# Kernel tuning notes

Measured on AMD Instinct MI355X. Metric: run time of the kernel, lower is better.

Reference implementation:

```python
import jax, jax.numpy as jnp
import numpy as np

B, EMBED, HEADS, T = 2, 512, 8, 2048
DH = EMBED // HEADS
EPS = 1e-5
# NOTE: torch code computes embed_dim // num_heads ** 0.5 == 512 // sqrt(8)
SCALE = EMBED // HEADS ** 0.5  # = 181.0, reproduced faithfully


def ws_conv1x1(x, w, b, mask):
    # weight-standardized 1x1 conv; w: [O, I], x: [B, I, T], mask: [B, T]
    mu = jnp.mean(w, axis=1, keepdims=True)
    var = jnp.var(w, axis=1, keepdims=True)
    wn = (w - mu) * jax.lax.rsqrt(var + EPS)
    x = x * mask[:, None, :].astype(x.dtype)
    return jnp.einsum('oi,bit->bot', wn, x) + b[None, :, None]


def ln_head(x, g, b):
    # per-head LayerNorm over head dim; x: [B, H, DH, T], normalized over DH
    xt = jnp.swapaxes(x, -1, -2)  # [B, H, T, DH]
    mu = jnp.mean(xt, axis=-1, keepdims=True)
    var = jnp.var(xt, axis=-1, keepdims=True)
    xn = (xt - mu) * jax.lax.rsqrt(var + EPS) * g + b
    return jnp.swapaxes(xn, -1, -2)


def setup_inputs():
    key = jax.random.key(0)
    ks = jax.random.split(key, 12)
    sc = 1.0 / np.sqrt(EMBED)
    d = {
        'q': jax.random.normal(ks[0], (B, EMBED, T), jnp.float32),
        'k': jax.random.normal(ks[1], (B, EMBED, T), jnp.float32),
        'v': jax.random.normal(ks[2], (B, EMBED, T), jnp.float32),
        'query_mask': jax.random.randint(ks[3], (B, T), 0, 2, jnp.int32),
        'key_mask': jax.random.randint(ks[4], (B, T), 0, 2, jnp.int32),
        'value_mask': jax.random.randint(ks[5], (B, T), 0, 2, jnp.int32),
        'Wq': jax.random.normal(ks[6], (EMBED, EMBED), jnp.float32) * sc,
        'bq': jnp.zeros((EMBED,), jnp.float32),
        'Wk': jax.random.normal(ks[7], (EMBED, EMBED), jnp.float32) * sc,
        'bk': jnp.zeros((EMBED,), jnp.float32),
        'Wv': jax.random.normal(ks[8], (EMBED, EMBED), jnp.float32) * sc,
        'bv': jnp.zeros((EMBED,), jnp.float32),
        'Wo': jax.random.normal(ks[9], (EMBED, EMBED), jnp.float32) * sc,
        'bo': jnp.zeros((EMBED,), jnp.float32),
        'ln_gq': jnp.ones((DH,), jnp.float32), 'ln_bq': jnp.zeros((DH,), jnp.float32),
        'ln_gk': jnp.ones((DH,), jnp.float32), 'ln_bk': jnp.zeros((DH,), jnp.float32),
        'ln_gv': jnp.ones((DH,), jnp.float32), 'ln_bv': jnp.zeros((DH,), jnp.float32),
    }
    return d


def reference(q, k, v, query_mask, key_mask, value_mask,
              Wq, bq, Wk, bk, Wv, bv, Wo, bo,
              ln_gq, ln_bq, ln_gk, ln_bk, ln_gv, ln_bv):
    q = ws_conv1x1(q, Wq, bq, query_mask)   # [B, E, T]
    k = ws_conv1x1(k, Wk, bk, key_mask)
    v = ws_conv1x1(v, Wv, bv, value_mask)
    # split heads: [B, E, T] -> [B, H, DH, T]
    q = q.reshape(B, HEADS, DH, T)
    k = k.reshape(B, HEADS, DH, T)
    v = v.reshape(B, HEADS, DH, T)
    # middle_norm: per-head LayerNorm over DH
    q = ln_head(q, ln_gq, ln_bq)
    k = ln_head(k, ln_gk, ln_bk)
    v = ln_head(v, ln_gv, ln_bv)
    # scores = q^T k / scale : [B, H, Tq, Tk]
    scores = jnp.einsum('bhdq,bhdk->bhqk', q, k) / SCALE
    scores = jnp.where(key_mask[:, None, None, :] == 0, -1e9, scores)
    scores = jax.nn.softmax(scores, axis=-1)
    scores = jnp.where(query_mask[:, None, :, None] == 0, 0.0, scores)
    # out = (scores @ v^T)^T : [B, H, DH, Tq]
    out = jnp.einsum('bhqk,bhdk->bhdq', scores, v)
    out = out.reshape(B, EMBED, T)
    out = ws_conv1x1(out, Wo, bo, query_mask)
    return out
```

## Files before the change

### kernel.cpp

```cpp
#include <hip/hip_runtime.h>


typedef __bf16 bf16;
typedef __bf16 bf16x2 __attribute__((ext_vector_type(2)));
typedef __bf16 bf16x8 __attribute__((ext_vector_type(8)));
typedef _Float16 f16;
typedef _Float16 f16x4 __attribute__((ext_vector_type(4)));
typedef _Float16 f16x8 __attribute__((ext_vector_type(8)));
typedef float  f32x4  __attribute__((ext_vector_type(4)));

#define MFMA_BF16(a, b, c) __builtin_amdgcn_mfma_f32_16x16x32_bf16((a), (b), (c), 0, 0, 0)
#define MFMA_F16_K32(a, b, c) __builtin_amdgcn_mfma_f32_16x16x32_f16((a), (b), (c), 0, 0, 0)

#if __has_builtin(__builtin_amdgcn_exp2f)
#define EXP2F(x) __builtin_amdgcn_exp2f(x)
#else
#define EXP2F(x) __expf((x) * 0.6931471805599453f)
#endif

#define NB   2
#define NE   512
#define NH   8
#define NT   2048
#define NDH  64

__device__ __forceinline__ void gl_lds16(const bf16* g, bf16* l) {
  __builtin_amdgcn_global_load_lds(
      (const __attribute__((address_space(1))) void*)g,
      (__attribute__((address_space(3))) void*)l, 16, 0, 0);
}

__global__ __launch_bounds__(64) void k_wstd(
    const float* __restrict__ Wq, const float* __restrict__ Wk,
    const float* __restrict__ Wv, const float* __restrict__ Wo,
    const int* __restrict__ km,
    bf16* __restrict__ out, f16* __restrict__ kmh)
{
  if (blockIdx.y == 4) {
    int idx = blockIdx.x * 64 + threadIdx.x;
    if (idx < NB * NT) kmh[idx] = (f16)(float)km[idx];
    return;
  }
  const float* W = blockIdx.y == 0 ? Wq : blockIdx.y == 1 ? Wk
                 : blockIdx.y == 2 ? Wv : Wo;
  int row = blockIdx.x, lane = threadIdx.x;
  const float4* p = (const float4*)(W + row * NE) + lane * 2;
  float4 a = p[0], c = p[1];
  float s  = a.x + a.y + a.z + a.w + c.x + c.y + c.z + c.w;
  float ss = a.x*a.x + a.y*a.y + a.z*a.z + a.w*a.w
           + c.x*c.x + c.y*c.y + c.z*c.z + c.w*c.w;
#pragma unroll
  for (int m = 1; m < 64; m <<= 1) { s += __shfl_xor(s, m); ss += __shfl_xor(ss, m); }
  float mean = s * (1.0f / NE);
  float var  = ss * (1.0f / NE) - mean * mean;
  float rstd = rsqrtf(var + 1e-5f);
  bf16x8 o;
  o[0] = (bf16)((a.x - mean) * rstd); o[1] = (bf16)((a.y - mean) * rstd);
  o[2] = (bf16)((a.z - mean) * rstd); o[3] = (bf16)((a.w - mean) * rstd);
  o[4] = (bf16)((c.x - mean) * rstd); o[5] = (bf16)((c.y - mean) * rstd);
  o[6] = (bf16)((c.z - mean) * rstd); o[7] = (bf16)((c.w - mean) * rstd);
  *(bf16x8*)(out + blockIdx.y * (NE * NE) + row * NE + lane * 8) = o;
}

__global__ __launch_bounds__(256) void k_trans(
    const float* __restrict__ q, const float* __restrict__ k,
    const float* __restrict__ v,
    const int* __restrict__ qm, const int* __restrict__ km,
    const int* __restrict__ vm,
    bf16* __restrict__ xT)
{
  int src = blockIdx.z >> 1, b = blockIdx.z & 1;
  const float* x = src == 0 ? q : src == 1 ? k : v;
  const int*   m = src == 0 ? qm : src == 1 ? km : vm;
  x += (size_t)b * NE * NT;
  m += b * NT;
  int t0 = blockIdx.x * 64, i0 = blockIdx.y * 64;
  __shared__ float tile[64][65];
  int lr = threadIdx.x >> 4;
  int tc = (threadIdx.x & 15) * 4;
#pragma unroll
  for (int p = 0; p < 4; p++) {
    int row = p * 16 + lr;
    float4 v4 = *(const float4*)(x + (size_t)(i0 + row) * NT + t0 + tc);
    tile[row][tc]     = v4.x; tile[row][tc + 1] = v4.y;
    tile[row][tc + 2] = v4.z; tile[row][tc + 3] = v4.w;
  }
  __syncthreads();
  bf16* o = xT + ((size_t)src * NB + b) * NT * NE;
  int i2 = (threadIdx.x & 31) * 2, t2 = threadIdx.x >> 5;
#pragma unroll
  for (int t = t2; t < 64; t += 8) {
    float mk = (float)m[t0 + t];
    bf16x2 w2;
    w2[0] = (bf16)(tile[i2][t] * mk);
    w2[1] = (bf16)(tile[i2 + 1][t] * mk);
    *(bf16x2*)(o + (size_t)(t0 + t) * NE + i0 + i2) = w2;
  }
}

__global__ __launch_bounds__(256) void k_proj(
    const bf16* __restrict__ Wn,
    const bf16* __restrict__ xT,
    const int* __restrict__ km,
    const float* __restrict__ bq, const float* __restrict__ bk,
    const float* __restrict__ bv,
    const float* __restrict__ gq, const float* __restrict__ bbq,
    const float* __restrict__ gk, const float* __restrict__ bbk,
    const float* __restrict__ gv, const float* __restrict__ bbv,
    bf16* __restrict__ Qh, bf16* __restrict__ Kh, f16* __restrict__ Vh)
{
  int src = blockIdx.z >> 1, b = blockIdx.z & 1;
  const bf16* A  = Wn + src * (NE * NE);
  const bf16* Bm = xT + ((size_t)src * NB + b) * NT * NE;
  int m0 = blockIdx.y * 64, n0 = blockIdx.x * 128;
  int h = m0 >> 6;

  __shared__ __align__(16) char smem[64 * 130 * 4 + 2 * 128 * 4];
  bf16*  Al = (bf16*)smem;
  bf16*  Bl = (bf16*)(smem + 8192);
  float* Yl = (float*)smem;
  float* mu = (float*)(smem + 64 * 130 * 4);
  float* rs = mu + 128;

  int tid = threadIdx.x, lane = tid & 63, w = tid >> 6;
  int mh = (w & 1) * 32, nh = (w >> 1) * 64;
  f32x4 acc[2][4] = {};

  for (int k0 = 0; k0 < NE; k0 += 64) {
    __syncthreads();
#pragma unroll
    for (int i = 0; i < 2; i++) {
      int row = (w << 4) + (i << 3) + (lane >> 3);
      int chg = (lane & 7) ^ (row & 7);
      gl_lds16(A + (m0 + row) * NE + k0 + (chg << 3),
               Al + ((w << 4) + (i << 3)) * 64);
    }
#pragma unroll
    for (int i = 0; i < 4; i++) {
      int row = (w << 5) + (i << 3) + (lane >> 3);
      int chg = (lane & 7) ^ (row & 7);
      gl_lds16(Bm + (size_t)(n0 + row) * NE + k0 + (chg << 3),
               Bl + ((w << 5) + (i << 3)) * 64);
    }
    __syncthreads();
#pragma unroll
    for (int kk = 0; kk < 64; kk += 32) {
      bf16x8 af[2], bfv[4];
#pragma unroll
      for (int ms = 0; ms < 2; ms++) {
        int row = mh + ms * 16 + (lane & 15);
        af[ms] = *(const bf16x8*)(Al + row * 64 +
                   ((((kk >> 3) + (lane >> 4)) ^ (row & 7)) << 3));
      }
#pragma unroll
      for (int ns = 0; ns < 4; ns++) {
        int row = nh + ns * 16 + (lane & 15);
        bfv[ns] = *(const bf16x8*)(Bl + row * 64 +
                   ((((kk >> 3) + (lane >> 4)) ^ (row & 7)) << 3));
      }
#pragma unroll
      for (int ms = 0; ms < 2; ms++)
#pragma unroll
        for (int ns = 0; ns < 4; ns++)
          acc[ms][ns] = MFMA_BF16(af[ms], bfv[ns], acc[ms][ns]);
    }
  }

  __syncthreads();
  {
    const float* bias = src == 0 ? bq : src == 1 ? bk : bv;
#pragma unroll
    for (int ms = 0; ms < 2; ms++)
#pragma unroll
      for (int ns = 0; ns < 4; ns++)
#pragma unroll
        for (int r = 0; r < 4; r++) {
          int om = mh + ms * 16 + ((lane >> 4) << 2) + r;
          int on = nh + ns * 16 + (lane & 15);
          Yl[om * 130 + on] = acc[ms][ns][r] + bias[m0 + om];
        }
  }
  __syncthreads();
  if (tid < 128) {
    float s = 0.f, ss = 0.f;
#pragma unroll 8
    for (int o = 0; o < 64; o++) { float y = Yl[o * 130 + tid]; s += y; ss += y * y; }
    float mean = s * (1.0f / 64.0f);
    float var  = ss * (1.0f / 64.0f) - mean * mean;
    mu[tid] = mean;
    rs[tid] = rsqrtf(var + 1e-5f);
  }
  __syncthreads();

  if (src < 2) {
    float scl = (src == 0) ? (1.4426950408889634f / 181.0f) : 1.0f;
    const float* g  = src == 0 ? gq  : gk;
    const float* bb = src == 0 ? bbq : bbk;
    bf16* out = (src == 0 ? Qh : Kh) + ((size_t)(b * NH + h) * NT + n0) * NDH;
    int d = tid & 63, tb = tid >> 6;
    float gg = g[d] * scl, bb2 = bb[d] * scl;
#pragma unroll
    for (int t = tb; t < 128; t += 4) {
      float val = (Yl[d * 130 + t] - mu[t]) * rs[t] * gg + bb2;
      out[(size_t)t * NDH + d] = (bf16)val;
    }
  } else {
    f16* out = Vh + (size_t)(b * NH + h) * NDH * NT + n0;
    int t = tid & 127, db = tid >> 7;
    float mk = (float)km[b * NT + n0 + t];
#pragma unroll
    for (int d = db; d < 64; d += 2) {
      float val = (Yl[d * 130 + t] - mu[t]) * rs[t] * gv[d] + bbv[d];
      out[(size_t)d * NT + t] = (f16)(val * mk);
    }
  }
}

__global__ __launch_bounds__(256) void k_attn(
    const bf16* __restrict__ Qh, const bf16* __restrict__ Kh,
    const f16* __restrict__ Vh, const f16* __restrict__ kmh,
    const int* __restrict__ qmask,
    bf16* __restrict__ xa)
{
  int bh = blockIdx.y, b = bh >> 3, h = bh & 7;
  int q0 = blockIdx.x * 64;
  const bf16* Q = Qh + (size_t)bh * NT * NDH;
  const bf16* K = Kh + (size_t)bh * NT * NDH;
  const f16*  V = Vh + (size_t)bh * NDH * NT;

  __shared__ __align__(16) char smem[2 * 64 * 68 * 4 + 4 * 64 * 4];
  float* OlA  = (float*)smem;
  float* OlB  = (float*)(smem + 64 * 68 * 4);
  float* denl = (float*)(smem + 2 * 64 * 68 * 4);

  int tid = threadIdx.x, lane = tid & 63, w = tid >> 6;
  int quad = lane >> 4, l15 = lane & 15;
  const int ko = w * 32;

  bf16x8 qb[4][2];
#pragma unroll
  for (int qs = 0; qs < 4; qs++)
#pragma unroll
    for (int hf = 0; hf < 2; hf++)
      qb[qs][hf] = *(const bf16x8*)(Q + (size_t)(q0 + qs * 16 + l15) * NDH + hf * 32 + quad * 8);

  const bf16* Kb = K + (size_t)(ko + l15) * NDH + quad * 8;
  const f16*  Vb = V + (size_t)l15 * NT + ko + quad * 4;
  const f16*  Mb = kmh + b * NT + ko + quad * 4;

  f32x4 acco[4][4] = {};
  f32x4 dacc[4]    = {};

  bf16x8 ka[2][2];
  f16x8  vb8[4];
  f16x8  kb8;
#pragma unroll
  for (int kt = 0; kt < 2; kt++)
#pragma unroll
    for (int hf = 0; hf < 2; hf++)
      ka[kt][hf] = *(const bf16x8*)(Kb + (size_t)(kt * 16) * NDH + hf * 32);
#pragma unroll
  for (int ds = 0; ds < 4; ds++) {
    f16x4 lo = *(const f16x4*)(Vb + (size_t)(ds * 16) * NT);
    f16x4 hi = *(const f16x4*)(Vb + (size_t)(ds * 16) * NT + 16);
    f16x8 vv;
    vv[0] = lo[0]; vv[1] = lo[1]; vv[2] = lo[2]; vv[3] = lo[3];
    vv[4] = hi[0]; vv[5] = hi[1]; vv[6] = hi[2]; vv[7] = hi[3];
    vb8[ds] = vv;
  }
  {
    f16x4 lo = *(const f16x4*)(Mb);
    f16x4 hi = *(const f16x4*)(Mb + 16);
    f16x8 vv;
    vv[0] = lo[0]; vv[1] = lo[1]; vv[2] = lo[2]; vv[3] = lo[3];
    vv[4] = hi[0]; vv[5] = hi[1]; vv[6] = hi[2]; vv[7] = hi[3];
    kb8 = vv;
  }

  for (int k0 = 0; k0 < NT; k0 += 128) {
    int k1 = (k0 + 128) & (NT - 1);
    bf16x8 nka[2][2];
    f16x8  nvb[4], nkb;
#pragma unroll
    for (int kt = 0; kt < 2; kt++)
#pragma unroll
      for (int hf = 0; hf < 2; hf++)
        nka[kt][hf] = *(const bf16x8*)(Kb + (size_t)(k1 + kt * 16) * NDH + hf * 32);
#pragma unroll
    for (int ds = 0; ds < 4; ds++) {
      f16x4 lo = *(const f16x4*)(Vb + (size_t)(ds * 16) * NT + k1);
      f16x4 hi = *(const f16x4*)(Vb + (size_t)(ds * 16) * NT + k1 + 16);
      f16x8 vv;
      vv[0] = lo[0]; vv[1] = lo[1]; vv[2] = lo[2]; vv[3] = lo[3];
      vv[4] = hi[0]; vv[5] = hi[1]; vv[6] = hi[2]; vv[7] = hi[3];
      nvb[ds] = vv;
    }
    {
      f16x4 lo = *(const f16x4*)(Mb + k1);
      f16x4 hi = *(const f16x4*)(Mb + k1 + 16);
      f16x8 vv;
      vv[0] = lo[0]; vv[1] = lo[1]; vv[2] = lo[2]; vv[3] = lo[3];
      vv[4] = hi[0]; vv[5] = hi[1]; vv[6] = hi[2]; vv[7] = hi[3];
      nkb = vv;
    }

#pragma unroll
    for (int qs = 0; qs < 4; qs++) {
      f32x4 z0 = {}, z1 = {};
      z0 = MFMA_BF16(ka[0][0], qb[qs][0], z0);
      z0 = MFMA_BF16(ka[0][1], qb[qs][1], z0);
      z1 = MFMA_BF16(ka[1][0], qb[qs][0], z1);
      z1 = MFMA_BF16(ka[1][1], qb[qs][1], z1);
      f16x8 pa;
#pragma unroll
      for (int r = 0; r < 4; r++) {
        pa[r]     = (f16)EXP2F(z0[r]);
        pa[4 + r] = (f16)EXP2F(z1[r]);
      }
      dacc[qs] = MFMA_F16_K32(pa, kb8, dacc[qs]);
#pragma unroll
      for (int ds = 0; ds < 4; ds++)
        acco[qs][ds] = MFMA_F16_K32(pa, vb8[ds], acco[qs][ds]);
    }

#pragma unroll
    for (int kt = 0; kt < 2; kt++)
#pragma unroll
      for (int hf = 0; hf < 2; hf++)
        ka[kt][hf] = nka[kt][hf];
#pragma unroll
    for (int ds = 0; ds < 4; ds++)
      vb8[ds] = nvb[ds];
    kb8 = nkb;
  }

  if (l15 == 0)
#pragma unroll
    for (int qs = 0; qs < 4; qs++)
#pragma unroll
      for (int r = 0; r < 4; r++)
        denl[w * 64 + qs * 16 + quad * 4 + r] = dacc[qs][r];

  float* Obuf = (w < 2) ? OlA : OlB;
  if ((w & 1) == 0) {
#pragma unroll
    for (int qs = 0; qs < 4; qs++)
#pragma unroll
      for (int ds = 0; ds < 4; ds++)
#pragma unroll
        for (int r = 0; r < 4; r++)
          Obuf[(qs * 16 + quad * 4 + r) * 68 + ds * 16 + l15] = acco[qs][ds][r];
  }
  __syncthreads();
  if (w & 1) {
#pragma unroll
    for (int qs = 0; qs < 4; qs++)
#pragma unroll
      for (int ds = 0; ds < 4; ds++)
#pragma unroll
        for (int r = 0; r < 4; r++)
          Obuf[(qs * 16 + quad * 4 + r) * 68 + ds * 16 + l15] += acco[qs][ds][r];
  }
  __syncthreads();

#pragma unroll
  for (int i = 0; i < 16; i++) {
    int ql = w * 16 + i;
    float dtot = denl[ql] + denl[64 + ql] + denl[128 + ql] + denl[192 + ql];
    float qm = (float)qmask[b * NT + q0 + ql];
    float inv = qm / dtot;
    float val = (OlA[ql * 68 + lane] + OlB[ql * 68 + lane]) * inv;
    xa[((size_t)b * NT + q0 + ql) * NE + h * NDH + lane] = (bf16)val;
  }
}

__global__ __launch_bounds__(256) void k_oproj(
    const bf16* __restrict__ A,
    const bf16* __restrict__ xab,
    const float* __restrict__ bo, float* __restrict__ out)
{
  int b = blockIdx.z;
  const bf16* Bm = xab + (size_t)b * NT * NE;
  int m0 = blockIdx.y * 64, n0 = blockIdx.x * 64;

  __shared__ __align__(16) char smem[16384];
  bf16* Al = (bf16*)smem;
  bf16* Bl = (bf16*)(smem + 8192);

  int tid = threadIdx.x, lane = tid & 63, w = tid >> 6;
  int mh = (w & 1) * 32, nh = (w >> 1) * 32;
  f32x4 acc[2][2] = {};

  for (int k0 = 0; k0 < NE; k0 += 64) {
    __syncthreads();
#pragma unroll
    for (int i = 0; i < 2; i++) {
      int row = (w << 4) + (i << 3) + (lane >> 3);
      int chg = (lane & 7) ^ (row & 7);
      gl_lds16(A + (m0 + row) * NE + k0 + (chg << 3),
               Al + ((w << 4) + (i << 3)) * 64);
    }
#pragma unroll
    for (int i = 0; i < 2; i++) {
      int row = (w << 4) + (i << 3) + (lane >> 3);
      int chg = (lane & 7) ^ (row & 7);
      gl_lds16(Bm + (size_t)(n0 + row) * NE + k0 + (chg << 3),
               Bl + ((w << 4) + (i << 3)) * 64);
    }
    __syncthreads();
#pragma unroll
    for (int kk = 0; kk < 64; kk += 32) {
      bf16x8 af[2], bfv[2];
#pragma unroll
      for (int ms = 0; ms < 2; ms++) {
        int row = mh + ms * 16 + (lane & 15);
        af[ms] = *(const bf16x8*)(Al + row * 64 +
                   ((((kk >> 3) + (lane >> 4)) ^ (row & 7)) << 3));
      }
#pragma unroll
      for (int ns = 0; ns < 2; ns++) {
        int row = nh + ns * 16 + (lane & 15);
        bfv[ns] = *(const bf16x8*)(Bl + row * 64 +
                   ((((kk >> 3) + (lane >> 4)) ^ (row & 7)) << 3));
      }
#pragma unroll
      for (int ms = 0; ms < 2; ms++)
#pragma unroll
        for (int ns = 0; ns < 2; ns++)
          acc[ms][ns] = MFMA_BF16(af[ms], bfv[ns], acc[ms][ns]);
    }
  }

#pragma unroll
  for (int ms = 0; ms < 2; ms++)
#pragma unroll
    for (int ns = 0; ns < 2; ns++)
#pragma unroll
      for (int r = 0; r < 4; r++) {
        int o = m0 + mh + ms * 16 + ((lane >> 4) << 2) + r;
        int t = n0 + nh + ns * 16 + (lane & 15);
        out[(size_t)b * NE * NT + (size_t)o * NT + t] = acc[ms][ns][r] + bo[o];
      }
}

extern "C" void kernel_launch(void* const* d_in, const int* in_sizes, int n_in,
                              void* d_out, int out_size, void* d_ws, size_t ws_size,
                              hipStream_t stream)
{
  const float* q  = (const float*)d_in[0];
  const float* k  = (const float*)d_in[1];
  const float* v  = (const float*)d_in[2];
  const int*   qm = (const int*)d_in[3];
  const int*   km = (const int*)d_in[4];
  const int*   vm = (const int*)d_in[5];
  const float* Wq = (const float*)d_in[6];  const float* bq = (const float*)d_in[7];
  const float* Wk = (const float*)d_in[8];  const float* bk = (const float*)d_in[9];
  const float* Wv = (const float*)d_in[10]; const float* bv = (const float*)d_in[11];
  const float* Wo = (const float*)d_in[12]; const float* bo = (const float*)d_in[13];
  const float* gq = (const float*)d_in[14]; const float* bbq = (const float*)d_in[15];
  const float* gk = (const float*)d_in[16]; const float* bbk = (const float*)d_in[17];
  const float* gv = (const float*)d_in[18]; const float* bbv = (const float*)d_in[19];
  float* out = (float*)d_out;

  char* wsb = (char*)d_ws;
  bf16*  Wn  = (bf16*)(wsb);
  bf16*  xT  = (bf16*)(wsb + (2ull  << 20));
  bf16*  Qh  = (bf16*)(wsb + (14ull << 20));
  bf16*  Kh  = (bf16*)(wsb + (18ull << 20));
  f16*   Vh  = (f16*) (wsb + (22ull << 20));
  bf16*  xa  = (bf16*)(wsb + (26ull << 20));
  f16*   kmh = (f16*) (wsb + (30ull << 20));

  k_wstd <<<dim3(512, 5),   64,  0, stream>>>(Wq, Wk, Wv, Wo, km, Wn, kmh);
  k_trans<<<dim3(32, 8, 6), 256, 0, stream>>>(q, k, v, qm, km, vm, xT);
  k_proj <<<dim3(16, 8, 6), 256, 0, stream>>>(Wn, xT, km, bq, bk, bv,
                                              gq, bbq, gk, bbk, gv, bbv,
                                              Qh, Kh, Vh);
  k_attn <<<dim3(32, 16),   256, 0, stream>>>(Qh, Kh, Vh, kmh, qm, xa);
  k_oproj<<<dim3(32, 8, 2), 256, 0, stream>>>(Wn + 3 * NE * NE, xa, bo, out);
}
```

Baseline: 183.3 us.

## Store V and key mask in MFMA fragment order for contiguous attention loads

The V projection epilogue now writes V, together with the key mask as a fifth fragment, directly in the per-lane MFMA operand layout. Each attention wave can then fetch its five f16x8 operands with single 16-byte loads instead of pairs of strided 8-byte loads plus lane shuffling. This also removes the separate key-mask conversion blocks from the weight-standardization kernel and reuses the xT workspace region for xa. The cost is a more scattered, less coalesced write pattern in the projection epilogue.

Result: faster. 170.9 us (-6.8%).

```diff
diff --git a/kernel.cpp b/kernel.cpp
--- a/kernel.cpp
+++ b/kernel.cpp
@@ -5,7 +5,6 @@
 typedef __bf16 bf16x2 __attribute__((ext_vector_type(2)));
 typedef __bf16 bf16x8 __attribute__((ext_vector_type(8)));
 typedef _Float16 f16;
-typedef _Float16 f16x4 __attribute__((ext_vector_type(4)));
 typedef _Float16 f16x8 __attribute__((ext_vector_type(8)));
 typedef float  f32x4  __attribute__((ext_vector_type(4)));
 
@@ -23,6 +22,7 @@
 #define NH   8
 #define NT   2048
 #define NDH  64
+#define VF_BH_STRIDE (64 * 5 * 64 * 8)
 
 __device__ __forceinline__ void gl_lds16(const bf16* g, bf16* l) {
   __builtin_amdgcn_global_load_lds(
@@ -33,14 +33,8 @@
 __global__ __launch_bounds__(64) void k_wstd(
     const float* __restrict__ Wq, const float* __restrict__ Wk,
     const float* __restrict__ Wv, const float* __restrict__ Wo,
-    const int* __restrict__ km,
-    bf16* __restrict__ out, f16* __restrict__ kmh)
-{
-  if (blockIdx.y == 4) {
-    int idx = blockIdx.x * 64 + threadIdx.x;
-    if (idx < NB * NT) kmh[idx] = (f16)(float)km[idx];
-    return;
-  }
+    bf16* __restrict__ out)
+{
   const float* W = blockIdx.y == 0 ? Wq : blockIdx.y == 1 ? Wk
                  : blockIdx.y == 2 ? Wv : Wo;
   int row = blockIdx.x, lane = threadIdx.x;
@@ -107,7 +101,7 @@
     const float* __restrict__ gq, const float* __restrict__ bbq,
     const float* __restrict__ gk, const float* __restrict__ bbk,
     const float* __restrict__ gv, const float* __restrict__ bbv,
-    bf16* __restrict__ Qh, bf16* __restrict__ Kh, f16* __restrict__ Vh)
+    bf16* __restrict__ Qh, bf16* __restrict__ Kh, f16* __restrict__ Vf)
 {
   int src = blockIdx.z >> 1, b = blockIdx.z & 1;
   const bf16* A  = Wn + src * (NE * NE);
@@ -205,28 +199,46 @@
       out[(size_t)t * NDH + d] = (bf16)val;
     }
   } else {
-    f16* out = Vh + (size_t)(b * NH + h) * NDH * NT + n0;
-    int t = tid & 127, db = tid >> 7;
-    float mk = (float)km[b * NT + n0 + t];
-#pragma unroll
-    for (int d = db; d < 64; d += 2) {
-      float val = (Yl[d * 130 + t] - mu[t]) * rs[t] * gv[d] + bbv[d];
-      out[(size_t)d * NT + t] = (f16)(val * mk);
-    }
+    int gl = tid >> 6, lane2 = tid & 63;
+    int quad2 = lane2 >> 4, l15b = lane2 & 15;
+    int bh = b * NH + h;
+    f16* base = Vf + (size_t)bh * VF_BH_STRIDE
+              + (size_t)((n0 >> 5) + gl) * (5 * 64 * 8) + lane2 * 8;
+    int   tl[8]; float mk[8];
+#pragma unroll
+    for (int j = 0; j < 8; j++) {
+      tl[j] = gl * 32 + ((j < 4) ? quad2 * 4 + j : 16 + quad2 * 4 + (j - 4));
+      mk[j] = (float)km[b * NT + n0 + tl[j]];
+    }
+#pragma unroll
+    for (int ds = 0; ds < 4; ds++) {
+      int d = ds * 16 + l15b;
+      float gg = gv[d], bb3 = bbv[d];
+      f16x8 o;
+#pragma unroll
+      for (int j = 0; j < 8; j++) {
+        int t = tl[j];
+        o[j] = (f16)(((Yl[d * 130 + t] - mu[t]) * rs[t] * gg + bb3) * mk[j]);
+      }
+      *(f16x8*)(base + ds * (64 * 8)) = o;
+    }
+    f16x8 om;
+#pragma unroll
+    for (int j = 0; j < 8; j++) om[j] = (f16)mk[j];
+    *(f16x8*)(base + 4 * (64 * 8)) = om;
   }
 }
 
 __global__ __launch_bounds__(256) void k_attn(
     const bf16* __restrict__ Qh, const bf16* __restrict__ Kh,
-    const f16* __restrict__ Vh, const f16* __restrict__ kmh,
-    const int* __restrict__ qmask,
+    const f16* __restrict__ Vf, const int* __restrict__ qmask,
     bf16* __restrict__ xa)
 {
   int bh = blockIdx.y, b = bh >> 3, h = bh & 7;
   int q0 = blockIdx.x * 64;
   const bf16* Q = Qh + (size_t)bh * NT * NDH;
   const bf16* K = Kh + (size_t)bh * NT * NDH;
-  const f16*  V = Vh + (size_t)bh * NDH * NT;
+  const f16*  VfB = Vf + (size_t)bh * VF_BH_STRIDE;
 
   __shared__ __align__(16) char smem[2 * 64 * 68 * 4 + 4 * 64 * 4];
   float* OlA  = (float*)smem;
@@ -245,64 +257,34 @@
       qb[qs][hf] = *(const bf16x8*)(Q + (size_t)(q0 + qs * 16 + l15) * NDH + hf * 32 + quad * 8);
 
   const bf16* Kb = K + (size_t)(ko + l15) * NDH + quad * 8;
-  const f16*  Vb = V + (size_t)l15 * NT + ko + quad * 4;
-  const f16*  Mb = kmh + b * NT + ko + quad * 4;
 
   f32x4 acco[4][4] = {};
   f32x4 dacc[4]    = {};
 
   bf16x8 ka[2][2];
-  f16x8  vb8[4];
-  f16x8  kb8;
+  f16x8  vb8[5];
 #pragma unroll
   for (int kt = 0; kt < 2; kt++)
 #pragma unroll
     for (int hf = 0; hf < 2; hf++)
       ka[kt][hf] = *(const bf16x8*)(Kb + (size_t)(kt * 16) * NDH + hf * 32);
 #pragma unroll
-  for (int ds = 0; ds < 4; ds++) {
-    f16x4 lo = *(const f16x4*)(Vb + (size_t)(ds * 16) * NT);
-    f16x4 hi = *(const f16x4*)(Vb + (size_t)(ds * 16) * NT + 16);
-    f16x8 vv;
-    vv[0] = lo[0]; vv[1] = lo[1]; vv[2] = lo[2]; vv[3] = lo[3];
-    vv[4] = hi[0]; vv[5] = hi[1]; vv[6] = hi[2]; vv[7] = hi[3];
-    vb8[ds] = vv;
-  }
-  {
-    f16x4 lo = *(const f16x4*)(Mb);
-    f16x4 hi = *(const f16x4*)(Mb + 16);
-    f16x8 vv;
-    vv[0] = lo[0]; vv[1] = lo[1]; vv[2] = lo[2]; vv[3] = lo[3];
-    vv[4] = hi[0]; vv[5] = hi[1]; vv[6] = hi[2]; vv[7] = hi[3];
-    kb8 = vv;
-  }
+  for (int j5 = 0; j5 < 5; j5++)
+    vb8[j5] = *(const f16x8*)(VfB + ((size_t)w * 5 + j5) * 512 + lane * 8);
 
   for (int k0 = 0; k0 < NT; k0 += 128) {
     int k1 = (k0 + 128) & (NT - 1);
+    int g1 = (k1 >> 5) + w;
     bf16x8 nka[2][2];
-    f16x8  nvb[4], nkb;
+    f16x8  nvb[5];
 #pragma unroll
     for (int kt = 0; kt < 2; kt++)
 #pragma unroll
       for (int hf = 0; hf < 2; hf++)
         nka[kt][hf] = *(const bf16x8*)(Kb + (size_t)(k1 + kt * 16) * NDH + hf * 32);
 #pragma unroll
-    for (int ds = 0; ds < 4; ds++) {
-      f16x4 lo = *(const f16x4*)(Vb + (size_t)(ds * 16) * NT + k1);
-      f16x4 hi = *(const f16x4*)(Vb + (size_t)(ds * 16) * NT + k1 + 16);
-      f16x8 vv;
-      vv[0] = lo[0]; vv[1] = lo[1]; vv[2] = lo[2]; vv[3] = lo[3];
-      vv[4] = hi[0]; vv[5] = hi[1]; vv[6] = hi[2]; vv[7] = hi[3];
-      nvb[ds] = vv;
-    }
-    {
-      f16x4 lo = *(const f16x4*)(Mb + k1);
-      f16x4 hi = *(const f16x4*)(Mb + k1 + 16);
-      f16x8 vv;
-      vv[0] = lo[0]; vv[1] = lo[1]; vv[2] = lo[2]; vv[3] = lo[3];
-      vv[4] = hi[0]; vv[5] = hi[1]; vv[6] = hi[2]; vv[7] = hi[3];
-      nkb = vv;
-    }
+    for (int j5 = 0; j5 < 5; j5++)
+      nvb[j5] = *(const f16x8*)(VfB + ((size_t)g1 * 5 + j5) * 512 + lane * 8);
 
 #pragma unroll
     for (int qs = 0; qs < 4; qs++) {
@@ -317,7 +299,7 @@
         pa[r]     = (f16)EXP2F(z0[r]);
         pa[4 + r] = (f16)EXP2F(z1[r]);
       }
-      dacc[qs] = MFMA_F16_K32(pa, kb8, dacc[qs]);
+      dacc[qs] = MFMA_F16_K32(pa, vb8[4], dacc[qs]);
 #pragma unroll
       for (int ds = 0; ds < 4; ds++)
         acco[qs][ds] = MFMA_F16_K32(pa, vb8[ds], acco[qs][ds]);
@@ -329,9 +311,8 @@
       for (int hf = 0; hf < 2; hf++)
         ka[kt][hf] = nka[kt][hf];
 #pragma unroll
-    for (int ds = 0; ds < 4; ds++)
-      vb8[ds] = nvb[ds];
-    kb8 = nkb;
+    for (int j5 = 0; j5 < 5; j5++)
+      vb8[j5] = nvb[j5];
   }
 
   if (l15 == 0)
@@ -465,17 +446,16 @@
   char* wsb = (char*)d_ws;
   bf16*  Wn  = (bf16*)(wsb);
   bf16*  xT  = (bf16*)(wsb + (2ull  << 20));
+  bf16*  xa  = (bf16*)(wsb + (2ull  << 20));
   bf16*  Qh  = (bf16*)(wsb + (14ull << 20));
   bf16*  Kh  = (bf16*)(wsb + (18ull << 20));
-  f16*   Vh  = (f16*) (wsb + (22ull << 20));
-  bf16*  xa  = (bf16*)(wsb + (26ull << 20));
-  f16*   kmh = (f16*) (wsb + (30ull << 20));
-
-  k_wstd <<<dim3(512, 5),   64,  0, stream>>>(Wq, Wk, Wv, Wo, km, Wn, kmh);
+  f16*   Vf  = (f16*) (wsb + (22ull << 20));
+
+  k_wstd <<<dim3(512, 4),   64,  0, stream>>>(Wq, Wk, Wv, Wo, Wn);
   k_trans<<<dim3(32, 8, 6), 256, 0, stream>>>(q, k, v, qm, km, vm, xT);
   k_proj <<<dim3(16, 8, 6), 256, 0, stream>>>(Wn, xT, km, bq, bk, bv,
                                               gq, bbq, gk, bbk, gv, bbv,
-                                              Qh, Kh, Vh);
-  k_attn <<<dim3(32, 16),   256, 0, stream>>>(Qh, Kh, Vh, kmh, qm, xa);
+                                              Qh, Kh, Vf);
+  k_attn <<<dim3(32, 16),   256, 0, stream>>>(Qh, Kh, Vf, qm, xa);
   k_oproj<<<dim3(32, 8, 2), 256, 0, stream>>>(Wn + 3 * NE * NE, xa, bo, out);
 }
```
